# Optimization experiments

Hardware: AMD Instinct MI355X
Metric: run time of the kernel (lower is better)

The kernel has to match this reference:

```python
import jax, jax.numpy as jnp
import numpy as np


def setup_inputs() -> dict:
    key = jax.random.key(0)
    kx, kh = jax.random.split(key)
    x = jax.random.normal(kx, (32, 4, 131072), dtype=jnp.float32)
    h = jax.random.normal(kh, (32, 4, 32768), dtype=jnp.float32)
    return {"x": x, "h": h}


def reference(x, h):
    # Causal FFT convolution: convolve(x, h, mode='causal', pad_mode='min').
    x_len = x.shape[-1]
    h_len = h.shape[-1]
    pad_len = x_len + h_len - 1  # pad_mode='min'
    # rfft with n=pad_len == zero-pad to pad_len then rfft (matches F.pad + rfft)
    X = jnp.fft.rfft(x, n=pad_len)
    H = jnp.fft.rfft(h, n=pad_len)
    Y = X * H
    # torch.fft.irfft default output length = 2*(n_freq-1); jnp matches this default.
    y_pad = jnp.fft.irfft(Y)
    # 'causal' mode: keep first x_len samples
    return y_pad[..., :x_len]
```

## Files before the change

kernel.cpp:

```cpp
#include <hip/hip_runtime.h>
#include <hip/hip_fp16.h>


#define L1FFT 262144
#define NCHAN 128
#define CN1 163839LL
#define CN2 163838LL
#define MBINS 81920
#define XLEN 131072
#define HLEN 32768
#define TWO_PI 6.28318530717958647692f
#define INV512T (1.0f/512.0f)
#define INVLT   (1.0f/262144.0f)
#define CHIRP12 ((float)(0.5 / (163839.0 * 163838.0)))

#define CM_BUILD 0
#define CM_REAL  1
#define CM_XCOMB 2
#define CM_FINAL 3
#define RM_BUILD 0
#define RM_CONV2 1
#define RM_CONVX 2

#define TS  518
#define TFS 261

typedef float cplx __attribute__((ext_vector_type(2)));

__device__ __forceinline__ cplx mkc(float x, float y){ cplx r; r.x = x; r.y = y; return r; }
__device__ __forceinline__ cplx cmulf(cplx a, cplx b) {
  return a.xx*b + a.yy*mkc(-b.y, b.x);
}
__device__ __forceinline__ cplx cmulcf(cplx a, cplx b) {
  return a.yy*b.yx + a.xx*mkc(b.x, -b.y);
}
__device__ __forceinline__ cplx crot(cplx t, float dsg) {
  return mkc(-dsg*t.y, dsg*t.x);
}

__device__ __forceinline__ cplx sc_turn(float t) {
  return mkc(__builtin_amdgcn_cosf(t), __builtin_amdgcn_sinf(t));
}

__device__ __forceinline__ cplx chirp1(float sgn, long long n) {
  long long m = (n*n) % (2*CN1);
  return sc_turn(sgn * (float)m * (1.0f/(float)(2*CN1)));
}
__device__ __forceinline__ cplx chirp2(float sgn, long long n) {
  long long m = (n*n) % (2*CN2);
  return sc_turn(sgn * (float)m * (1.0f/(float)(2*CN2)));
}
__device__ __forceinline__ cplx chirpv(float sgn, long long Q, long long n) {
  long long m = (n*n) % (2*Q);
  float ang = sgn * (0.5f*TWO_PI) * (float)m / (float)Q;
  float s, c; __sincosf(ang, &s, &c);
  return mkc(c, s);
}

__device__ __forceinline__ int brev4(int x) {
  return ((x&1)<<3) | ((x&2)<<1) | ((x&4)>>1) | ((x&8)>>3);
}
__device__ __forceinline__ int brev5(int x) {
  return (int)(__brev((unsigned)x) >> 27);
}

template<int M>
__device__ __forceinline__ float shf1f(float x) {
  if constexpr (M == 1) {
    return __int_as_float(__builtin_amdgcn_mov_dpp(__float_as_int(x), 0xB1, 0xF, 0xF, true));
  } else if constexpr (M == 2) {
    return __int_as_float(__builtin_amdgcn_mov_dpp(__float_as_int(x), 0x4E, 0xF, 0xF, true));
  } else if constexpr (M == 8) {
    return __int_as_float(__builtin_amdgcn_mov_dpp(__float_as_int(x), 0x128, 0xF, 0xF, true));
  } else {
    return __int_as_float(__builtin_amdgcn_ds_swizzle(__float_as_int(x), (M << 10) | 0x1F));
  }
}
template<int M>
__device__ __forceinline__ cplx shflxT(cplx a) {
  return mkc(shf1f<M>(a.x), shf1f<M>(a.y));
}

__device__ __forceinline__ cplx h2c(__half2 h) {
  float2 f = __half22float2(h); return mkc(f.x, f.y);
}
__device__ __forceinline__ __half2 c2h(cplx c) {
  return __float22half2_rn(make_float2(c.x, c.y));
}

#define C16_1 0.9238795325f
#define C16_2 0.7071067812f
#define C16_3 0.3826834324f
__device__ __forceinline__ float c16t(int j) {
  const float C[8] = {1.f, C16_1, C16_2, C16_3, 0.f, -C16_3, -C16_2, -C16_1};
  return C[j];
}
__device__ __forceinline__ float s16t(int j) {
  const float S[8] = {0.f, C16_3, C16_2, C16_1, 1.f, C16_1, C16_2, C16_3};
  return S[j];
}

__device__ __forceinline__ void lane16_fwd_rest(cplx v[16], float dsg) {
  #pragma unroll
  for (int h = 0; h < 2; ++h)
    #pragma unroll
    for (int j = 0; j < 4; ++j) {
      int i0 = h*8 + j;
      cplx w = mkc(c16t(2*j), dsg * s16t(2*j));
      cplx a = v[i0], b = v[i0+4];
      v[i0] = a + b;
      v[i0+4] = cmulf(a - b, w);
    }
  #pragma unroll
  for (int q = 0; q < 4; ++q)
    #pragma unroll
    for (int j = 0; j < 2; ++j) {
      int i0 = q*4 + j;
      cplx a = v[i0], b = v[i0+2];
      cplx tt = a - b;
      v[i0] = a + b;
      v[i0+2] = (j == 0) ? tt : crot(tt, dsg);
    }
  #pragma unroll
  for (int p = 0; p < 8; ++p) {
    cplx a = v[2*p], b = v[2*p+1];
    v[2*p] = a + b;
    v[2*p+1] = a - b;
  }
}
__device__ __forceinline__ void lane16_fwd(cplx v[16], float dsg) {
  #pragma unroll
  for (int j = 0; j < 8; ++j) {
    cplx w = mkc(c16t(j), dsg * s16t(j));
    cplx a = v[j], b = v[j+8];
    v[j] = a + b;
    v[j+8] = cmulf(a - b, w);
  }
  lane16_fwd_rest(v, dsg);
}
__device__ __forceinline__ void lane16_fwd_h0(cplx v[16], float dsg) {
  #pragma unroll
  for (int j = 0; j < 8; ++j) {
    cplx w = mkc(c16t(j), dsg * s16t(j));
    v[j+8] = cmulf(v[j], w);
  }
  lane16_fwd_rest(v, dsg);
}

__device__ __forceinline__ void lane16_inv(cplx v[16], float dsg) {
  #pragma unroll
  for (int p = 0; p < 8; ++p) {
    cplx a = v[2*p], b = v[2*p+1];
    v[2*p] = a + b;
    v[2*p+1] = a - b;
  }
  #pragma unroll
  for (int q = 0; q < 4; ++q)
    #pragma unroll
    for (int j = 0; j < 2; ++j) {
      int i0 = q*4 + j;
      cplx a = v[i0], b = v[i0+2];
      cplx tb = (j == 0) ? b : crot(b, -dsg);
      v[i0] = a + tb;
      v[i0+2] = a - tb;
    }
  #pragma unroll
  for (int h = 0; h < 2; ++h)
    #pragma unroll
    for (int j = 0; j < 4; ++j) {
      int i0 = h*8 + j;
      cplx w = mkc(c16t(2*j), dsg * s16t(2*j));
      cplx a = v[i0], b = v[i0+4];
      cplx tb = cmulcf(b, w);
      v[i0] = a + tb;
      v[i0+4] = a - tb;
    }
  #pragma unroll
  for (int j = 0; j < 8; ++j) {
    cplx w = mkc(c16t(j), dsg * s16t(j));
    cplx a = v[j], b = v[j+8];
    cplx tb = cmulcf(b, w);
    v[j] = a + tb;
    v[j+8] = a - tb;
  }
}

struct WSel { cplx a16, a8, a4, a2; };
__device__ __forceinline__ WSel make_wsel(int l, float dsg) {
  const cplx one = mkc(1.f, 0.f);
  WSel w;
  w.a16 = (l & 16) ? sc_turn(dsg * (1.0f/32.0f) * (float)(l & 15)) : one;
  w.a8  = (l & 8)  ? sc_turn(dsg * (1.0f/16.0f) * (float)(l & 7))  : one;
  w.a4  = (l & 4)  ? sc_turn(dsg * (1.0f/8.0f)  * (float)(l & 3))  : one;
  w.a2  = ((l & 2) && (l & 1)) ? mkc(0.f, dsg) : one;
  return w;
}

#define XF(mask, w) {                                                          \
    const float s_ = ((l & (mask)) != 0) ? -1.f : 1.f;                         \
    _Pragma("unroll")                                                          \
    for (int r = 0; r < 16; ++r) {                                             \
      cplx o = shflxT<(mask)>(v[r]);                                           \
      v[r] = cmulf(o + s_*v[r], (w));                                          \
    } }
#define XFP(mask) {                                                            \
    const float s_ = ((l & (mask)) != 0) ? -1.f : 1.f;                         \
    _Pragma("unroll")                                                          \
    for (int r = 0; r < 16; ++r) {                                             \
      cplx o = shflxT<(mask)>(v[r]);                                           \
      v[r] = o + s_*v[r];                                                      \
    } }
#define XI(mask, w) {                                                          \
    const float s_ = ((l & (mask)) != 0) ? -1.f : 1.f;                         \
    _Pragma("unroll")                                                          \
    for (int r = 0; r < 16; ++r) {                                             \
      cplx b = cmulcf(v[r], (w));                                              \
      cplx o = shflxT<(mask)>(b);                                              \
      v[r] = o + s_*b;                                                         \
    } }
#define XIP(mask) {                                                            \
    const float s_ = ((l & (mask)) != 0) ? -1.f : 1.f;                         \
    _Pragma("unroll")                                                          \
    for (int r = 0; r < 16; ++r) {                                             \
      cplx b = v[r];                                                           \
      cplx o = shflxT<(mask)>(b);                                              \
      v[r] = o + s_*b;                                                         \
    } }

#define TW_APPLY_FWD(rr, wexpr) v[rr] = cmulf(v[rr], (wexpr));
#define TW_APPLY_INV(rr, wexpr) v[rr] = cmulcf(v[rr], (wexpr));
#define TW512_BODY(APPLY)                                                      \
  cplx w1 = sc_turn(dsg * INV512T * (float)l);                                 \
  cplx w2 = cmulf(w1, w1);                                                     \
  cplx w3 = cmulf(w2, w1);                                                     \
  cplx w4 = cmulf(w2, w2);                                                     \
  cplx w8 = cmulf(w4, w4);                                                     \
  cplx w12 = cmulf(w8, w4);                                                    \
  APPLY(8, w1)  APPLY(4, w2)  APPLY(12, w3) APPLY(2, w4)                       \
  APPLY(10, cmulf(w4, w1)) APPLY(6, cmulf(w4, w2)) APPLY(14, cmulf(w4, w3))    \
  APPLY(1, w8)  APPLY(9, cmulf(w8, w1)) APPLY(5, cmulf(w8, w2))                \
  APPLY(13, cmulf(w8, w3)) APPLY(3, w12) APPLY(11, cmulf(w12, w1))             \
  APPLY(7, cmulf(w12, w2)) APPLY(15, cmulf(w12, w3))

__device__ __forceinline__ void twiddle512_fwd(cplx v[16], int l, float dsg) {
  TW512_BODY(TW_APPLY_FWD)
}
__device__ __forceinline__ void twiddle512_inv(cplx v[16], int l, float dsg) {
  TW512_BODY(TW_APPLY_INV)
}

__device__ __forceinline__ void fft512_core_fwd(cplx v[16], int l, float dsg,
                                                const WSel& w) {
  twiddle512_fwd(v, l, dsg);
  XF(16, w.a16); XF(8, w.a8); XF(4, w.a4); XF(2, w.a2); XFP(1);
}
__device__ __forceinline__ void fft512_fwd(cplx v[16], int l, float dsg,
                                           const WSel& w) {
  lane16_fwd(v, dsg);
  fft512_core_fwd(v, l, dsg, w);
}
__device__ __forceinline__ void fft512_fwd_h0(cplx v[16], int l, float dsg,
                                              const WSel& w) {
  lane16_fwd_h0(v, dsg);
  fft512_core_fwd(v, l, dsg, w);
}

__device__ __forceinline__ void fft512_inv(cplx v[16], int l, float dsg,
                                           const WSel& w) {
  XIP(1); XI(2, w.a2); XI(4, w.a4); XI(8, w.a8); XI(16, w.a16);
  twiddle512_inv(v, l, dsg);
  lane16_inv(v, dsg);
}


__device__ __forceinline__ void gather_tile(__half2* tile, const __half2* src,
                                            int c0, int t) {
  const uint2* srcp = (const uint2*)src;
  #pragma unroll
  for (int i = 0; i < 8; ++i) {
    int qq = t + 256*i;
    int cc = qq & 7, rp = qq >> 3;
    *(uint2*)&tile[cc*TS + 2*rp] = srcp[(size_t)rp*512 + c0 + cc];
  }
}
__device__ __forceinline__ void scatter_tile(__half2* dst, const __half2* tile,
                                             int c0, int t) {
  uint2* dstp = (uint2*)dst;
  #pragma unroll
  for (int i = 0; i < 8; ++i) {
    int qq = t + 256*i;
    int cc = qq & 7, rp = qq >> 3;
    dstp[(size_t)rp*512 + c0 + cc] = *(const uint2*)&tile[cc*TS + 2*rp];
  }
}

__device__ __forceinline__ void twiddle_store(__half2* tile, cplx v[16],
                                              int l, int ccf, int c) {
  cplx B1 = sc_turn(-INVLT * (float)c);
  cplx C  = sc_turn(-INVLT * (float)(c * (16*brev5(l))));
  cplx B2 = cmulf(B1, B1);
  cplx B4 = cmulf(B2, B2);
  cplx d0 = C, d1 = cmulf(C, B1), d2 = cmulf(C, B2), d3 = cmulf(d1, B2);
  #define ST4(r0,r1,r2,r3)                                                     \
    tile[ccf*TS + l + 32*(r0)] = c2h(cmulf(v[r0], d0));                        \
    tile[ccf*TS + l + 32*(r1)] = c2h(cmulf(v[r1], d1));                        \
    tile[ccf*TS + l + 32*(r2)] = c2h(cmulf(v[r2], d2));                        \
    tile[ccf*TS + l + 32*(r3)] = c2h(cmulf(v[r3], d3));
  #define DUP4()                                                               \
    d0 = cmulf(d0, B4); d1 = cmulf(d1, B4);                                    \
    d2 = cmulf(d2, B4); d3 = cmulf(d3, B4);
  ST4(0, 8, 4, 12)  DUP4()
  ST4(2, 10, 6, 14) DUP4()
  ST4(1, 9, 5, 13)  DUP4()
  ST4(3, 11, 7, 15)
  #undef ST4
  #undef DUP4
}

__global__ __launch_bounds__(256) void pass_col_k(
    int mode,
    const float* __restrict__ realA, int lenA,
    const float* __restrict__ realB, int lenB,
    const __half2* srcX, const __half2* srcH,
    __half2* dstFull,
    float* __restrict__ realOut,
    int nc, int chunkSlots,
    long long Qa, float csgnA, int loA, int hiA,
    long long Qb, float csgnB, int loB, int hiB)
{
  __shared__ __align__(16) unsigned char ldsraw[8 * TS * 4];
  __half2* tile = (__half2*)ldsraw;
  const int t   = threadIdx.x;
  const int c0  = blockIdx.x * 8;
  const int y   = blockIdx.y;
  const int l   = t & 31;
  const int ccf = t >> 5;
  const int c   = c0 + ccf;
  cplx v[16];
  WSel ws = make_wsel(l, -1.f);

  if (mode == CM_BUILD) {
    long long Q = (y == 0) ? Qa : Qb;
    float csgn  = (y == 0) ? csgnA : csgnB;
    int lo = (y == 0) ? loA : loB;
    int hi = (y == 0) ? hiA : hiB;
    #pragma unroll
    for (int m = 0; m < 16; ++m) {
      int n = ((l + 32*m) << 9) + c;
      int np = (n <= hi) ? n : n - L1FFT;
      v[m] = (np >= lo) ? chirpv(csgn, Q, (long long)np) : mkc(0.f, 0.f);
    }
    fft512_fwd(v, l, -1.f, ws);
    twiddle_store(tile, v, l, ccf, c);
    __syncthreads();
    scatter_tile(dstFull + (size_t)y * L1FFT, tile, c0, t);
    return;
  }

  if (mode == CM_REAL) {
    const float* rs_; int rl_; int slot;
    if (y < nc) { rs_ = realA + (size_t)y * lenA;        rl_ = lenA; slot = y; }
    else        { rs_ = realB + (size_t)(y - nc) * lenB; rl_ = lenB;
                  slot = chunkSlots + (y - nc); }
    #pragma unroll
    for (int i = 0; i < 8; ++i) {
      int qq = t + 256*i;
      int cc = qq & 7, r = qq >> 3;
      int n = (r << 9) + c0 + cc;
      cplx val = mkc(0.f, 0.f);
      if (n < rl_) val = chirp1(-1.f, (long long)n) * rs_[n];
      tile[cc*TS + r] = c2h(val);
    }
    __syncthreads();
    #pragma unroll
    for (int m = 0; m < 8; ++m) v[m] = h2c(tile[ccf*TS + l + 32*m]);
    __syncthreads();
    fft512_fwd_h0(v, l, -1.f, ws);
    twiddle_store(tile, v, l, ccf, c);
    __syncthreads();
    scatter_tile(dstFull + (size_t)slot * L1FFT, tile, c0, t);
    return;
  }

  if (mode == CM_XCOMB) {
    gather_tile(tile, srcH + (size_t)y * L1FFT, c0, t);
    __syncthreads();
    #pragma unroll
    for (int m = 0; m < 16; ++m) v[m] = h2c(tile[ccf*TS + l + 32*m]);
    __syncthreads();
    fft512_inv(v, l, -1.f, ws);
    cplx Hf[5];
    #pragma unroll
    for (int m = 0; m <= 4; ++m) {
      int n = l + 32*m;
      long long k = ((long long)n << 9) + c;
      cplx cw = chirp1(-1.f, k);
      float fk = (float)k;
      cplx wc = sc_turn(fk * fk * CHIRP12);
      float eps = (k == 0 || k == MBINS-1) ? 1.f : 2.f;
      float sc = eps / (float)CN2;
      Hf[m] = cmulf(v[m], cmulf(cw, wc) * sc);
    }
    gather_tile(tile, srcX + (size_t)(chunkSlots + y) * L1FFT, c0, t);
    __syncthreads();
    #pragma unroll
    for (int m = 0; m < 16; ++m) v[m] = h2c(tile[ccf*TS + l + 32*m]);
    __syncthreads();
    fft512_inv(v, l, -1.f, ws);
    #pragma unroll
    for (int m = 0; m <= 4; ++m) v[m] = cmulf(v[m], Hf[m]);
    #pragma unroll
    for (int m = 5; m < 8; ++m) v[m] = mkc(0.f, 0.f);
    fft512_fwd_h0(v, l, -1.f, ws);
    twiddle_store(tile, v, l, ccf, c);
    __syncthreads();
    scatter_tile(dstFull + (size_t)(chunkSlots + y) * L1FFT, tile, c0, t);
    return;
  }

  gather_tile(tile, srcX + (size_t)(chunkSlots + y) * L1FFT, c0, t);
  __syncthreads();
  #pragma unroll
  for (int m = 0; m < 16; ++m) v[m] = h2c(tile[ccf*TS + l + 32*m]);
  __syncthreads();
  fft512_inv(v, l, -1.f, ws);
  float* tf = (float*)ldsraw;
  #pragma unroll
  for (int m = 0; m < 8; ++m) {
    int n = l + 32*m;
    long long nb = ((long long)n << 9) + c;
    cplx cw = chirp2(+1.f, nb);
    tf[ccf*TFS + n] = v[m].x*cw.x - v[m].y*cw.y;
  }
  __syncthreads();
  {
    int cc = t & 7, u = t >> 3;
    #pragma unroll
    for (int i = 0; i < 8; ++i) {
      int n = u + 32*i;
      realOut[(size_t)y*XLEN + (n << 9) + c0 + cc] = tf[cc*TFS + n];
    }
  }
}

__global__ __launch_bounds__(256) void pass_row_k(
    int mode, __half2* a, const __half2* __restrict__ g, int nc, int chunkSlots)
{
  const int t = threadIdx.x;
  const int l = t & 31;
  const int w8 = t >> 5;
  const int rs = blockIdx.x * 8 + w8;
  const int rp = rs >> 1, par = rs & 1;
  const int y = blockIdx.y;
  int slot;
  if (mode == RM_BUILD)      slot = y;
  else if (mode == RM_CONV2) slot = (y < nc) ? y : chunkSlots + (y - nc);
  else                       slot = chunkSlots + y;
  const int j = 16*brev5(rs & 31) + brev4(rs >> 5);
  __half2* A = a + (size_t)slot * L1FFT + (size_t)rp * 1024 + 2*l + par;
  cplx v[16];
  WSel ws = make_wsel(l, -1.f);
  #pragma unroll
  for (int m = 0; m < 16; ++m) v[m] = h2c(A[64*m]);

  if (mode != RM_BUILD) {
    const __half2* G = g + (size_t)rp * 1024 + 2*l + par;
    cplx gv[16];
    #pragma unroll
    for (int m = 0; m < 16; ++m) gv[m] = h2c(G[64*m]);
    fft512_fwd(v, l, -1.f, ws);
    #pragma unroll
    for (int r = 0; r < 16; ++r) v[r] = cmulf(v[r], gv[r]);
    fft512_inv(v, l, -1.f, ws);
    {
      cplx T = sc_turn(INVLT * (float)(l * j)) * (1.f/(float)L1FFT);
      cplx F = sc_turn(INVLT * (float)(32 * j));
      #pragma unroll
      for (int m = 0; m < 16; ++m) {
        A[64*m] = c2h(cmulf(v[m], T));
        T = cmulf(T, F);
      }
    }
  } else {
    fft512_fwd(v, l, -1.f, ws);
    #pragma unroll
    for (int r = 0; r < 16; ++r) A[64*r] = c2h(v[r]);
  }
}

__global__ void diag_ws_too_small(float* out) { out[0] = 123456.0f; }

extern "C" void kernel_launch(void* const* d_in, const int* in_sizes, int n_in,
                              void* d_out, int out_size, void* d_ws, size_t ws_size,
                              hipStream_t stream) {
  const float* x = (const float*)d_in[0];
  const float* h = (const float*)d_in[1];
  float* out = (float*)d_out;

  const size_t fixedB   = 2ull * L1FFT * sizeof(__half2);
  const size_t perChanB = 2ull * L1FFT * sizeof(__half2);
  if (ws_size < fixedB + perChanB) {
    diag_ws_too_small<<<1, 1, 0, stream>>>(out);
    return;
  }
  int chunk = (int)((ws_size - fixedB) / perChanB);
  if (chunk > NCHAN) chunk = NCHAN;

  __half2* V1 = (__half2*)d_ws;
  __half2* W  = V1 + L1FFT;
  __half2* A  = W + L1FFT;

  dim3 blk(256);

  pass_col_k<<<dim3(64, 2), blk, 0, stream>>>(CM_BUILD,
      nullptr, 0, nullptr, 0, nullptr, nullptr, V1, nullptr, 0, 0,
      CN1, +1.f, -(XLEN-1), MBINS-1,
      CN2, -1.f, -(MBINS-1), XLEN-1);
  pass_row_k<<<dim3(64, 2), blk, 0, stream>>>(RM_BUILD, V1, nullptr, 0, 0);

  for (int ch0 = 0; ch0 < NCHAN; ch0 += chunk) {
    int nc = NCHAN - ch0; if (nc > chunk) nc = chunk;
    const float* hq = h   + (size_t)ch0 * HLEN;
    const float* xq = x   + (size_t)ch0 * XLEN;
    float*       oq = out + (size_t)ch0 * XLEN;

    pass_col_k<<<dim3(64, 2*nc), blk, 0, stream>>>(CM_REAL,
        hq, HLEN, xq, XLEN, nullptr, nullptr, A, nullptr, nc, chunk,
        0, 0.f, 0, 0, 0, 0.f, 0, 0);
    pass_row_k<<<dim3(64, 2*nc), blk, 0, stream>>>(RM_CONV2, A, V1, nc, chunk);
    pass_col_k<<<dim3(64, nc), blk, 0, stream>>>(CM_XCOMB,
        nullptr, 0, nullptr, 0, A, A, A, nullptr, nc, chunk,
        0, 0.f, 0, 0, 0, 0.f, 0, 0);
    pass_row_k<<<dim3(64, nc), blk, 0, stream>>>(RM_CONVX, A, W, nc, chunk);
    pass_col_k<<<dim3(64, nc), blk, 0, stream>>>(CM_FINAL,
        nullptr, 0, nullptr, 0, A, nullptr, nullptr, oq, nc, chunk,
        0, 0.f, 0, 0, 0, 0.f, 0, 0);
  }
}
```

Baseline: 857.2 us.

## Split combine pass into extract and combine kernels; use permlane16 swap for stride-16 stage

The old XCOMB column pass ran two inverse 512-FFTs per block, one for the H spectrum and one for the X spectrum. It is now split: a new EXTRACT pass computes the chirp-scaled H spectrum into a half-precision buffer, and a COMBINE pass reads it back and multiplies it into X. Each kernel then does less work per block, which may lower register pressure, at the cost of an extra launch and a global round trip. Separately, the stride-16 butterfly stage uses permlane16_swap on paired registers instead of ds_swizzle when the builtin exists, and a __syncthreads is added before the final LDS reuse.

```diff
diff --git a/kernel.cpp b/kernel.cpp
--- a/kernel.cpp
+++ b/kernel.cpp
@@ -14,16 +14,23 @@
 #define INVLT   (1.0f/262144.0f)
 #define CHIRP12 ((float)(0.5 / (163839.0 * 163838.0)))
 
-#define CM_BUILD 0
-#define CM_REAL  1
-#define CM_XCOMB 2
-#define CM_FINAL 3
+#define CM_BUILD   0
+#define CM_REAL    1
+#define CM_COMBINE 2
+#define CM_EXTRACT 3
+#define CM_FINAL   4
 #define RM_BUILD 0
 #define RM_CONV2 1
 #define RM_CONVX 2
 
 #define TS  518
 #define TFS 261
+
+#if __has_builtin(__builtin_amdgcn_permlane16_swap)
+#define PL16 1
+#else
+#define PL16 0
+#endif
 
 typedef float cplx __attribute__((ext_vector_type(2)));
 
@@ -81,6 +88,33 @@
   return mkc(shf1f<M>(a.x), shf1f<M>(a.y));
 }
 
+#if PL16
+__device__ __forceinline__ void swap16c(cplx& a, cplx& b) {
+  float ax = a.x, bx = b.x, ay = a.y, by = b.y;
+  auto rx = __builtin_amdgcn_permlane16_swap(__float_as_uint(ax),
+                                             __float_as_uint(bx), false, false);
+  auto ry = __builtin_amdgcn_permlane16_swap(__float_as_uint(ay),
+                                             __float_as_uint(by), false, false);
+  a = mkc(__uint_as_float(rx[0]), __uint_as_float(ry[0]));
+  b = mkc(__uint_as_float(rx[1]), __uint_as_float(ry[1]));
+}
+__device__ __forceinline__ void xf16_pair(cplx& p, cplx& q, cplx wf) {
+  swap16c(p, q);
+  cplx add = p + q;
+  cplx sub = cmulf(p - q, wf);
+  swap16c(add, sub);
+  p = add; q = sub;
+}
+__device__ __forceinline__ void xi16_pair(cplx& p, cplx& q, cplx wf) {
+  swap16c(p, q);
+  cplx t = cmulcf(q, wf);
+  cplx add = p + t;
+  cplx sub = p - t;
+  swap16c(add, sub);
+  p = add; q = sub;
+}
+#endif
+
 __device__ __forceinline__ cplx h2c(__half2 h) {
   float2 f = __half22float2(h); return mkc(f.x, f.y);
 }
@@ -189,7 +223,7 @@
 __device__ __forceinline__ WSel make_wsel(int l, float dsg) {
   const cplx one = mkc(1.f, 0.f);
   WSel w;
-  w.a16 = (l & 16) ? sc_turn(dsg * (1.0f/32.0f) * (float)(l & 15)) : one;
+  w.a16 = sc_turn(dsg * (1.0f/32.0f) * (float)(l & 15));
   w.a8  = (l & 8)  ? sc_turn(dsg * (1.0f/16.0f) * (float)(l & 7))  : one;
   w.a4  = (l & 4)  ? sc_turn(dsg * (1.0f/8.0f)  * (float)(l & 3))  : one;
   w.a2  = ((l & 2) && (l & 1)) ? mkc(0.f, dsg) : one;
@@ -252,7 +286,13 @@
 __device__ __forceinline__ void fft512_core_fwd(cplx v[16], int l, float dsg,
                                                 const WSel& w) {
   twiddle512_fwd(v, l, dsg);
-  XF(16, w.a16); XF(8, w.a8); XF(4, w.a4); XF(2, w.a2); XFP(1);
+#if PL16
+  #pragma unroll
+  for (int r = 0; r < 16; r += 2) xf16_pair(v[r], v[r+1], w.a16);
+#else
+  { cplx w16 = (l & 16) ? w.a16 : mkc(1.f, 0.f); XF(16, w16); }
+#endif
+  XF(8, w.a8); XF(4, w.a4); XF(2, w.a2); XFP(1);
 }
 __device__ __forceinline__ void fft512_fwd(cplx v[16], int l, float dsg,
                                            const WSel& w) {
@@ -267,7 +307,13 @@
 
 __device__ __forceinline__ void fft512_inv(cplx v[16], int l, float dsg,
                                            const WSel& w) {
-  XIP(1); XI(2, w.a2); XI(4, w.a4); XI(8, w.a8); XI(16, w.a16);
+  XIP(1); XI(2, w.a2); XI(4, w.a4); XI(8, w.a8);
+#if PL16
+  #pragma unroll
+  for (int r = 0; r < 16; r += 2) xi16_pair(v[r], v[r+1], w.a16);
+#else
+  { cplx w16 = (l & 16) ? w.a16 : mkc(1.f, 0.f); XI(16, w16); }
+#endif
   twiddle512_inv(v, l, dsg);
   lane16_inv(v, dsg);
 }
@@ -321,8 +367,10 @@
     int mode,
     const float* __restrict__ realA, int lenA,
     const float* __restrict__ realB, int lenB,
-    const __half2* srcX, const __half2* srcH,
+    const __half2* cplxSrc,
+    const __half2* __restrict__ hcIn,
     __half2* dstFull,
+    __half2* __restrict__ specOut,
     float* __restrict__ realOut,
     int nc, int chunkSlots,
     long long Qa, float csgnA, int loA, int hiA,
@@ -382,14 +430,35 @@
     return;
   }
 
-  if (mode == CM_XCOMB) {
-    gather_tile(tile, srcH + (size_t)y * L1FFT, c0, t);
+  if (mode == CM_COMBINE) {
+    gather_tile(tile, cplxSrc + (size_t)(chunkSlots + y) * L1FFT, c0, t);
     __syncthreads();
     #pragma unroll
     for (int m = 0; m < 16; ++m) v[m] = h2c(tile[ccf*TS + l + 32*m]);
     __syncthreads();
     fft512_inv(v, l, -1.f, ws);
-    cplx Hf[5];
+    #pragma unroll
+    for (int m = 0; m <= 4; ++m) {
+      int n = l + 32*m;
+      cplx H = h2c(hcIn[(size_t)y*MBINS + c*160 + n]);
+      v[m] = cmulf(v[m], H);
+    }
+    #pragma unroll
+    for (int m = 5; m < 8; ++m) v[m] = mkc(0.f, 0.f);
+    fft512_fwd_h0(v, l, -1.f, ws);
+    twiddle_store(tile, v, l, ccf, c);
+    __syncthreads();
+    scatter_tile(dstFull + (size_t)(chunkSlots + y) * L1FFT, tile, c0, t);
+    return;
+  }
+
+  if (mode == CM_EXTRACT) {
+    gather_tile(tile, cplxSrc + (size_t)y * L1FFT, c0, t);
+    __syncthreads();
+    #pragma unroll
+    for (int m = 0; m < 16; ++m) v[m] = h2c(tile[ccf*TS + l + 32*m]);
+    __syncthreads();
+    fft512_inv(v, l, -1.f, ws);
     #pragma unroll
     for (int m = 0; m <= 4; ++m) {
       int n = l + 32*m;
@@ -399,32 +468,20 @@
       cplx wc = sc_turn(fk * fk * CHIRP12);
       float eps = (k == 0 || k == MBINS-1) ? 1.f : 2.f;
       float sc = eps / (float)CN2;
-      Hf[m] = cmulf(v[m], cmulf(cw, wc) * sc);
-    }
-    gather_tile(tile, srcX + (size_t)(chunkSlots + y) * L1FFT, c0, t);
-    __syncthreads();
-    #pragma unroll
-    for (int m = 0; m < 16; ++m) v[m] = h2c(tile[ccf*TS + l + 32*m]);
-    __syncthreads();
-    fft512_inv(v, l, -1.f, ws);
-    #pragma unroll
-    for (int m = 0; m <= 4; ++m) v[m] = cmulf(v[m], Hf[m]);
-    #pragma unroll
-    for (int m = 5; m < 8; ++m) v[m] = mkc(0.f, 0.f);
-    fft512_fwd_h0(v, l, -1.f, ws);
-    twiddle_store(tile, v, l, ccf, c);
-    __syncthreads();
-    scatter_tile(dstFull + (size_t)(chunkSlots + y) * L1FFT, tile, c0, t);
+      cplx cw2 = cmulf(cw, wc) * sc;
+      specOut[(size_t)y*MBINS + c*160 + n] = c2h(cmulf(v[m], cw2));
+    }
     return;
   }
 
-  gather_tile(tile, srcX + (size_t)(chunkSlots + y) * L1FFT, c0, t);
+  gather_tile(tile, cplxSrc + (size_t)(chunkSlots + y) * L1FFT, c0, t);
   __syncthreads();
   #pragma unroll
   for (int m = 0; m < 16; ++m) v[m] = h2c(tile[ccf*TS + l + 32*m]);
   __syncthreads();
   fft512_inv(v, l, -1.f, ws);
   float* tf = (float*)ldsraw;
+  __syncthreads();
   #pragma unroll
   for (int m = 0; m < 8; ++m) {
     int n = l + 32*m;
@@ -498,7 +555,8 @@
   float* out = (float*)d_out;
 
   const size_t fixedB   = 2ull * L1FFT * sizeof(__half2);
-  const size_t perChanB = 2ull * L1FFT * sizeof(__half2);
+  const size_t perChanB = 2ull * L1FFT * sizeof(__half2)
+                        + (size_t)MBINS * sizeof(__half2);
   if (ws_size < fixedB + perChanB) {
     diag_ws_too_small<<<1, 1, 0, stream>>>(out);
     return;
@@ -509,11 +567,12 @@
   __half2* V1 = (__half2*)d_ws;
   __half2* W  = V1 + L1FFT;
   __half2* A  = W + L1FFT;
+  __half2* Hc = A + 2ull * chunk * L1FFT;
 
   dim3 blk(256);
 
   pass_col_k<<<dim3(64, 2), blk, 0, stream>>>(CM_BUILD,
-      nullptr, 0, nullptr, 0, nullptr, nullptr, V1, nullptr, 0, 0,
+      nullptr, 0, nullptr, 0, nullptr, nullptr, V1, nullptr, nullptr, 0, 0,
       CN1, +1.f, -(XLEN-1), MBINS-1,
       CN2, -1.f, -(MBINS-1), XLEN-1);
   pass_row_k<<<dim3(64, 2), blk, 0, stream>>>(RM_BUILD, V1, nullptr, 0, 0);
@@ -525,15 +584,18 @@
     float*       oq = out + (size_t)ch0 * XLEN;
 
     pass_col_k<<<dim3(64, 2*nc), blk, 0, stream>>>(CM_REAL,
-        hq, HLEN, xq, XLEN, nullptr, nullptr, A, nullptr, nc, chunk,
+        hq, HLEN, xq, XLEN, nullptr, nullptr, A, nullptr, nullptr, nc, chunk,
         0, 0.f, 0, 0, 0, 0.f, 0, 0);
     pass_row_k<<<dim3(64, 2*nc), blk, 0, stream>>>(RM_CONV2, A, V1, nc, chunk);
-    pass_col_k<<<dim3(64, nc), blk, 0, stream>>>(CM_XCOMB,
-        nullptr, 0, nullptr, 0, A, A, A, nullptr, nc, chunk,
+    pass_col_k<<<dim3(64, nc), blk, 0, stream>>>(CM_EXTRACT,
+        nullptr, 0, nullptr, 0, A, nullptr, nullptr, Hc, nullptr, nc, chunk,
+        0, 0.f, 0, 0, 0, 0.f, 0, 0);
+    pass_col_k<<<dim3(64, nc), blk, 0, stream>>>(CM_COMBINE,
+        nullptr, 0, nullptr, 0, A, Hc, A, nullptr, nullptr, nc, chunk,
         0, 0.f, 0, 0, 0, 0.f, 0, 0);
     pass_row_k<<<dim3(64, nc), blk, 0, stream>>>(RM_CONVX, A, W, nc, chunk);
     pass_col_k<<<dim3(64, nc), blk, 0, stream>>>(CM_FINAL,
-        nullptr, 0, nullptr, 0, A, nullptr, nullptr, oq, nc, chunk,
+        nullptr, 0, nullptr, 0, A, nullptr, nullptr, nullptr, oq, nc, chunk,
         0, 0.f, 0, 0, 0, 0.f, 0, 0);
   }
 }
```

New measurement: 881.8 us. 1.03x slower.
